# Optimization experiments

Hardware: AMD Instinct MI355X
Metric: run time of the kernel (lower is better)

The kernel has to match this reference:

```python
import jax, jax.numpy as jnp
import numpy as np

N_NODES = 50000
N_EDGES = 800000
IN_DIM = 100
HID = 128
OUT = 128
EPS = 1e-5


def setup_inputs() -> dict:
    key = jax.random.key(0)
    ks = jax.random.split(key, 12)
    x = jax.random.normal(ks[0], (N_NODES, IN_DIM), dtype=jnp.float32)
    edge_index = jax.random.randint(ks[1], (2, N_EDGES), 0, N_NODES, dtype=jnp.int32)
    def lin(k, i, o):
        return jax.random.normal(k, (i, o), dtype=jnp.float32) * (1.0 / np.sqrt(i))
    return {
        "x": x,
        "edge_index": edge_index,
        "W_l0": lin(ks[2], IN_DIM, HID),  # neighbor transform, layer 0
        "b_l0": jnp.zeros((HID,), jnp.float32),
        "W_r0": lin(ks[3], IN_DIM, HID),  # root transform, layer 0
        "gamma0": jnp.ones((HID,), jnp.float32),
        "beta0": jnp.zeros((HID,), jnp.float32),
        "W_l1": lin(ks[4], HID, OUT),
        "b_l1": jnp.zeros((OUT,), jnp.float32),
        "W_r1": lin(ks[5], HID, OUT),
        "gamma1": jnp.ones((OUT,), jnp.float32),
        "beta1": jnp.zeros((OUT,), jnp.float32),
    }


def _sage_conv(x, edge_index, W_l, b_l, W_r):
    # PyG SAGEConv (mean aggr): out = lin_l(mean_{j->i} x_j) + lin_r(x_i)
    src, dst = edge_index[0], edge_index[1]
    n = x.shape[0]
    msg_sum = jax.ops.segment_sum(x[src], dst, num_segments=n)        # [N, d_in]
    cnt = jax.ops.segment_sum(jnp.ones((src.shape[0],), x.dtype), dst, num_segments=n)
    agg = msg_sum / jnp.maximum(cnt, 1.0)[:, None]
    return agg @ W_l + b_l + x @ W_r


def _batch_norm(x, gamma, beta):
    # BatchNorm1d with batch statistics (training-mode math, biased var)
    mean = x.mean(axis=0)
    var = x.var(axis=0)
    return gamma * (x - mean) / jnp.sqrt(var + EPS) + beta


def reference(x, edge_index, W_l0, b_l0, W_r0, gamma0, beta0, W_l1, b_l1, W_r1, gamma1, beta1):
    # Layer 0: SAGEConv -> BN -> ReLU (dropout off for determinism)
    h = _sage_conv(x, edge_index, W_l0, b_l0, W_r0)
    h = jax.nn.relu(_batch_norm(h, gamma0, beta0))
    # Layer 1 (last): SAGEConv -> BN
    h = _sage_conv(h, edge_index, W_l1, b_l1, W_r1)
    return _batch_norm(h, gamma1, beta1)
```

## Files before the change

### kernel.cpp

```cpp
#include <hip/hip_runtime.h>
#include <hip/hip_bf16.h>

#define N_NODES 50000
#define N_EDGES 800000
#define NPAD    50048
#define IN_DIM  100
#define HID     128
#define BN_EPS  1e-5f

#define BSHIFT  6
#define BUCKS   782
#define BSTRIDE 2048
#define BCAP    2048
#define NSLICE  16

typedef unsigned int uint;
typedef unsigned short u16;
typedef __attribute__((ext_vector_type(8))) unsigned short us8;
typedef __attribute__((ext_vector_type(8))) short s8;
typedef __attribute__((ext_vector_type(16))) float f16v;

__device__ __forceinline__ u16 f2bf(float f) {
    uint u = __builtin_bit_cast(uint, f);
    uint r = (u + 0x7FFFu + ((u >> 16) & 1u)) >> 16;
    return (u16)r;
}
__device__ __forceinline__ uint pack2(float a, float b) {
    return (uint)f2bf(a) | ((uint)f2bf(b) << 16);
}
__device__ __forceinline__ float bflo(uint p) { return __builtin_bit_cast(float, p << 16); }
__device__ __forceinline__ float bfhi(uint p) { return __builtin_bit_cast(float, p & 0xFFFF0000u); }

__global__ void init_cursor(int* __restrict__ bcursor) {
    int b = blockIdx.x * 256 + threadIdx.x;
    if (b < BUCKS) bcursor[b] = b * BSTRIDE;
}

__global__ __launch_bounds__(1024) void bucket_scatter_blk(
    const int* __restrict__ src, const int* __restrict__ dst,
    int* __restrict__ bcursor, uint* __restrict__ ebuf) {
    __shared__ int h[BUCKS];
    __shared__ int gb[BUCKS];
    int t = threadIdx.x;
    for (int i = t; i < BUCKS; i += 1024) h[i] = 0;
    __syncthreads();
    int base = blockIdx.x * 8192;
    int myb[8]; uint myv[8];
    #pragma unroll
    for (int r = 0; r < 8; ++r) {
        int e = base + r * 1024 + t;
        int b = -1; uint val = 0;
        if (e < N_EDGES) {
            int d = dst[e];
            b = d >> BSHIFT;
            val = (uint)src[e] | ((uint)(d & 63) << 16);
            atomicAdd(&h[b], 1);
        }
        myb[r] = b; myv[r] = val;
    }
    __syncthreads();
    for (int i = t; i < BUCKS; i += 1024) {
        int c = h[i];
        gb[i] = c ? atomicAdd(&bcursor[i], c) : 0;
        h[i] = 0;
    }
    __syncthreads();
    #pragma unroll
    for (int r = 0; r < 8; ++r) {
        int b = myb[r];
        if (b >= 0) {
            int pos = gb[b] + atomicAdd(&h[b], 1);
            ebuf[pos] = myv[r];
        }
    }
}

__global__ void cast_x_kernel(const float* __restrict__ x, u16* __restrict__ xb) {
    int idx = blockIdx.x * blockDim.x + threadIdx.x;
    if (idx >= NPAD * 128) return;
    int row = idx >> 7, k = idx & 127;
    float v = (row < N_NODES && k < IN_DIM) ? x[row * IN_DIM + k] : 0.f;
    xb[idx] = f2bf(v);
}

__global__ void cast_w_kernel(const float* __restrict__ W_l0, const float* __restrict__ W_r0,
                              const float* __restrict__ W_l1, const float* __restrict__ W_r1,
                              u16* __restrict__ d) {
    int w = blockIdx.y;
    const float* s = (w == 0) ? W_l0 : (w == 1) ? W_r0 : (w == 2) ? W_l1 : W_r1;
    int Ks = (w < 2) ? IN_DIM : HID;
    int idx = blockIdx.x * 256 + threadIdx.x;
    int n = idx >> 7, k = idx & 127;
    float v = (k < Ks) ? s[k * 128 + n] : 0.f;
    d[w * 16384 + idx] = f2bf(v);
}

template <int WRITE_BF16>
__global__ __launch_bounds__(512) void agg_gemm(
    const uint* __restrict__ ebuf, const int* __restrict__ bcursor,
    const u16* __restrict__ X,
    const u16* __restrict__ WtL, const u16* __restrict__ WtR,
    const float* __restrict__ bias,
    float* __restrict__ outf, u16* __restrict__ outb,
    float* __restrict__ gstats) {
    __shared__ u16 Aagg[64][136];
    __shared__ uint eL[BCAP];
    __shared__ u16 srcL[BCAP];
    __shared__ int cnt[64], ro[65], cur[64];
    __shared__ float s1L[128], s2L[128];

    int b = blockIdx.x;
    int t = threadIdx.x;
    int row0 = b * 64;
    int wave = t >> 6, lane = t & 63;
    int quad = lane >> 4, sub = lane & 15;

    int n = bcursor[b] - b * BSTRIDE;
    if (n > BCAP) n = BCAP;
    if (t < 64) cnt[t] = 0;
    if (t < 128) { s1L[t] = 0.f; s2L[t] = 0.f; }
    __syncthreads();
    for (int i = t; i < n; i += 512) {
        uint p = ebuf[b * BSTRIDE + i];
        eL[i] = p;
        atomicAdd(&cnt[p >> 16], 1);
    }
    __syncthreads();
    if (t < 64) {
        int v = cnt[t];
        int s = v;
        #pragma unroll
        for (int off = 1; off < 64; off <<= 1) {
            int u = __shfl_up(s, off, 64);
            if (t >= off) s += u;
        }
        ro[t] = s - v;
        cur[t] = s - v;
        if (t == 63) ro[64] = s;
    }
    __syncthreads();
    for (int i = t; i < n; i += 512) {
        uint p = eL[i];
        int pos = atomicAdd(&cur[p >> 16], 1);
        srcL[pos] = (u16)(p & 0xFFFFu);
    }
    __syncthreads();

    #pragma unroll
    for (int ni = 0; ni < 8; ++ni) {
        int nl = wave * 8 + ni;
        int node = row0 + nl;
        if (node >= N_NODES) {
            if (quad == 0) *(uint4*)&Aagg[nl][sub * 8] = make_uint4(0, 0, 0, 0);
            continue;
        }
        int rb = ro[nl], re = ro[nl + 1];
        float a0 = 0.f, a1 = 0.f, a2 = 0.f, a3 = 0.f;
        float a4 = 0.f, a5 = 0.f, a6 = 0.f, a7 = 0.f;
        int e = rb;
        for (; e + 16 <= re; e += 16) {
            int s0 = srcL[e + quad];
            int s1 = srcL[e + 4 + quad];
            int s2 = srcL[e + 8 + quad];
            int s3 = srcL[e + 12 + quad];
            uint4 v0 = ((const uint4*)(X + (size_t)s0 * 128))[sub];
            uint4 v1 = ((const uint4*)(X + (size_t)s1 * 128))[sub];
            uint4 v2 = ((const uint4*)(X + (size_t)s2 * 128))[sub];
            uint4 v3 = ((const uint4*)(X + (size_t)s3 * 128))[sub];
            a0 += (bflo(v0.x) + bflo(v1.x)) + (bflo(v2.x) + bflo(v3.x));
            a1 += (bfhi(v0.x) + bfhi(v1.x)) + (bfhi(v2.x) + bfhi(v3.x));
            a2 += (bflo(v0.y) + bflo(v1.y)) + (bflo(v2.y) + bflo(v3.y));
            a3 += (bfhi(v0.y) + bfhi(v1.y)) + (bfhi(v2.y) + bfhi(v3.y));
            a4 += (bflo(v0.z) + bflo(v1.z)) + (bflo(v2.z) + bflo(v3.z));
            a5 += (bfhi(v0.z) + bfhi(v1.z)) + (bfhi(v2.z) + bfhi(v3.z));
            a6 += (bflo(v0.w) + bflo(v1.w)) + (bflo(v2.w) + bflo(v3.w));
            a7 += (bfhi(v0.w) + bfhi(v1.w)) + (bfhi(v2.w) + bfhi(v3.w));
        }
        for (; e + 8 <= re; e += 8) {
            int s0 = srcL[e + quad];
            int s1 = srcL[e + 4 + quad];
            uint4 v0 = ((const uint4*)(X + (size_t)s0 * 128))[sub];
            uint4 v1 = ((const uint4*)(X + (size_t)s1 * 128))[sub];
            a0 += bflo(v0.x) + bflo(v1.x);
            a1 += bfhi(v0.x) + bfhi(v1.x);
            a2 += bflo(v0.y) + bflo(v1.y);
            a3 += bfhi(v0.y) + bfhi(v1.y);
            a4 += bflo(v0.z) + bflo(v1.z);
            a5 += bfhi(v0.z) + bfhi(v1.z);
            a6 += bflo(v0.w) + bflo(v1.w);
            a7 += bfhi(v0.w) + bfhi(v1.w);
        }
        for (; e < re; e += 4) {
            int ee = e + quad;
            if (ee < re) {
                int s0 = srcL[ee];
                uint4 v0 = ((const uint4*)(X + (size_t)s0 * 128))[sub];
                a0 += bflo(v0.x); a1 += bfhi(v0.x);
                a2 += bflo(v0.y); a3 += bfhi(v0.y);
                a4 += bflo(v0.z); a5 += bfhi(v0.z);
                a6 += bflo(v0.w); a7 += bfhi(v0.w);
            }
        }
        #pragma unroll
        for (int m = 16; m <= 32; m <<= 1) {
            a0 += __shfl_xor(a0, m, 64); a1 += __shfl_xor(a1, m, 64);
            a2 += __shfl_xor(a2, m, 64); a3 += __shfl_xor(a3, m, 64);
            a4 += __shfl_xor(a4, m, 64); a5 += __shfl_xor(a5, m, 64);
            a6 += __shfl_xor(a6, m, 64); a7 += __shfl_xor(a7, m, 64);
        }
        if (quad == 0) {
            float inv = 1.0f / fmaxf((float)(re - rb), 1.0f);
            uint4 o;
            o.x = pack2(a0 * inv, a1 * inv);
            o.y = pack2(a2 * inv, a3 * inv);
            o.z = pack2(a4 * inv, a5 * inv);
            o.w = pack2(a6 * inv, a7 * inv);
            *(uint4*)&Aagg[nl][sub * 8] = o;
        }
    }
    __syncthreads();

    int m31 = lane & 31;
    int kh  = lane >> 5;
    int rm = (wave & 1) * 32;
    int cn = (wave >> 1) * 32;
    f16v acc = (f16v)0.f;

    {
        s8 a_nxt = *(const s8*)&Aagg[rm + m31][kh * 8];
        s8 b_nxt = *(const s8*)(WtL + (cn + m31) * 128 + kh * 8);
        #pragma unroll
        for (int ks = 0; ks < 8; ++ks) {
            s8 a_cur = a_nxt, b_cur = b_nxt;
            if (ks < 7) {
                a_nxt = *(const s8*)&Aagg[rm + m31][(ks + 1) * 16 + kh * 8];
                b_nxt = *(const s8*)(WtL + (cn + m31) * 128 + (ks + 1) * 16 + kh * 8);
            }
            acc = __builtin_amdgcn_mfma_f32_32x32x16_bf16(a_cur, b_cur, acc, 0, 0, 0);
        }
    }
    {
        const u16* xrow = X + (size_t)(row0 + rm + m31) * 128;
        s8 a_nxt = *(const s8*)(xrow + kh * 8);
        s8 b_nxt = *(const s8*)(WtR + (cn + m31) * 128 + kh * 8);
        #pragma unroll
        for (int ks = 0; ks < 8; ++ks) {
            s8 a_cur = a_nxt, b_cur = b_nxt;
            if (ks < 7) {
                a_nxt = *(const s8*)(xrow + (ks + 1) * 16 + kh * 8);
                b_nxt = *(const s8*)(WtR + (cn + m31) * 128 + (ks + 1) * 16 + kh * 8);
            }
            acc = __builtin_amdgcn_mfma_f32_32x32x16_bf16(a_cur, b_cur, acc, 0, 0, 0);
        }
    }

    {
        int col = cn + m31;
        float bv = bias[col];
        float s1 = 0.f, s2 = 0.f;
        #pragma unroll
        for (int reg = 0; reg < 16; ++reg) {
            int rowin = (reg & 3) + 8 * (reg >> 2) + 4 * kh;
            int row = row0 + rm + rowin;
            if (row < N_NODES) {
                float v = acc[reg] + bv;
                if (WRITE_BF16)
                    outb[(size_t)row * 128 + col] = f2bf(v);
                else
                    outf[(size_t)row * 128 + col] = v;
                s1 += v;
                s2 = fmaf(v, v, s2);
            }
        }
        s1 += __shfl_xor(s1, 32, 64);
        s2 += __shfl_xor(s2, 32, 64);
        if (lane < 32) {
            atomicAdd(&s1L[col], s1);
            atomicAdd(&s2L[col], s2);
        }
    }
    __syncthreads();
    int slice = b & (NSLICE - 1);
    if (t < 128) {
        atomicAdd(&gstats[slice * 256 + t], s1L[t]);
        atomicAdd(&gstats[slice * 256 + 128 + t], s2L[t]);
    }
}

__global__ void bn_relu_inplace(u16* __restrict__ hb,
                                const float* __restrict__ gstats,
                                const float* __restrict__ gamma,
                                const float* __restrict__ beta,
                                float inv_n, int totalv) {
    __shared__ float ss[256];
    int t = threadIdx.x;
    if (t < 128) {
        float m = 0.f, q = 0.f;
        #pragma unroll
        for (int s = 0; s < NSLICE; ++s) {
            m += gstats[s * 256 + t];
            q += gstats[s * 256 + 128 + t];
        }
        float mean = m * inv_n;
        float var = q * inv_n - mean * mean;
        float inv = 1.0f / sqrtf(var + BN_EPS);
        float sc = gamma[t] * inv;
        ss[t] = sc;
        ss[128 + t] = beta[t] - mean * sc;
    }
    __syncthreads();
    for (int i = blockIdx.x * 256 + t; i < totalv; i += gridDim.x * 256) {
        int cg = (i & 15) * 8;
        uint4 p = ((const uint4*)hb)[i];
        float4 scA = *(const float4*)&ss[cg];
        float4 scB = *(const float4*)&ss[cg + 4];
        float4 shA = *(const float4*)&ss[128 + cg];
        float4 shB = *(const float4*)&ss[128 + cg + 4];
        float r0 = fmaxf(fmaf(bflo(p.x), scA.x, shA.x), 0.f);
        float r1 = fmaxf(fmaf(bfhi(p.x), scA.y, shA.y), 0.f);
        float r2 = fmaxf(fmaf(bflo(p.y), scA.z, shA.z), 0.f);
        float r3 = fmaxf(fmaf(bfhi(p.y), scA.w, shA.w), 0.f);
        float r4 = fmaxf(fmaf(bflo(p.z), scB.x, shB.x), 0.f);
        float r5 = fmaxf(fmaf(bfhi(p.z), scB.y, shB.y), 0.f);
        float r6 = fmaxf(fmaf(bflo(p.w), scB.z, shB.z), 0.f);
        float r7 = fmaxf(fmaf(bfhi(p.w), scB.w, shB.w), 0.f);
        uint4 o;
        o.x = pack2(r0, r1);
        o.y = pack2(r2, r3);
        o.z = pack2(r4, r5);
        o.w = pack2(r6, r7);
        ((uint4*)hb)[i] = o;
    }
}

__global__ void bn_apply_kernel(float* __restrict__ h,
                                const float* __restrict__ gstats,
                                const float* __restrict__ gamma,
                                const float* __restrict__ beta,
                                float inv_n, int total4) {
    __shared__ float ss[256];
    int t = threadIdx.x;
    if (t < 128) {
        float m = 0.f, q = 0.f;
        #pragma unroll
        for (int s = 0; s < NSLICE; ++s) {
            m += gstats[s * 256 + t];
            q += gstats[s * 256 + 128 + t];
        }
        float mean = m * inv_n;
        float var = q * inv_n - mean * mean;
        float inv = 1.0f / sqrtf(var + BN_EPS);
        float sc = gamma[t] * inv;
        ss[t] = sc;
        ss[128 + t] = beta[t] - mean * sc;
    }
    __syncthreads();
    for (int i = blockIdx.x * 256 + t; i < total4; i += gridDim.x * 256) {
        int cg = i & 31;
        float4 v = ((float4*)h)[i];
        float4 sc = *(const float4*)&ss[cg * 4];
        float4 sh = *(const float4*)&ss[128 + cg * 4];
        v.x = fmaf(v.x, sc.x, sh.x);
        v.y = fmaf(v.y, sc.y, sh.y);
        v.z = fmaf(v.z, sc.z, sh.z);
        v.w = fmaf(v.w, sc.w, sh.w);
        ((float4*)h)[i] = v;
    }
}

extern "C" void kernel_launch(void* const* d_in, const int* in_sizes, int n_in,
                              void* d_out, int out_size, void* d_ws, size_t ws_size,
                              hipStream_t stream) {
    const float* x      = (const float*)d_in[0];
    const int*   ei     = (const int*)d_in[1];
    const float* W_l0   = (const float*)d_in[2];
    const float* b_l0   = (const float*)d_in[3];
    const float* W_r0   = (const float*)d_in[4];
    const float* gamma0 = (const float*)d_in[5];
    const float* beta0  = (const float*)d_in[6];
    const float* W_l1   = (const float*)d_in[7];
    const float* b_l1   = (const float*)d_in[8];
    const float* W_r1   = (const float*)d_in[9];
    const float* gamma1 = (const float*)d_in[10];
    const float* beta1  = (const float*)d_in[11];

    const int* src = ei;
    const int* dst = ei + N_EDGES;

    char* w = (char*)d_ws;
    auto alloc = [&](size_t bytes) {
        void* p = (void*)w;
        w += (bytes + 255) & ~(size_t)255;
        return p;
    };
    char* zbase    = w;
    float* gstats0 = (float*)alloc(sizeof(float) * NSLICE * 256);
    float* gstats1 = (float*)alloc(sizeof(float) * NSLICE * 256);
    size_t zbytes  = (size_t)(w - zbase);

    int* bcursor   = (int*)alloc(sizeof(int) * BUCKS);
    uint* ebuf     = (uint*)alloc(sizeof(uint) * BUCKS * BSTRIDE);
    u16* xb        = (u16*)alloc(sizeof(u16) * (size_t)NPAD * 128);
    u16* hb        = (u16*)alloc(sizeof(u16) * (size_t)NPAD * 128);
    u16* Wt        = (u16*)alloc(sizeof(u16) * 4 * 16384);
    float* outp    = (float*)d_out;

    hipMemsetAsync(zbase, 0, zbytes, stream);

    const float inv_n = 1.0f / (float)N_NODES;
    const int total4 = N_NODES * HID / 4;
    const int totalv = N_NODES * HID / 8;

    init_cursor<<<(BUCKS + 255) / 256, 256, 0, stream>>>(bcursor);
    bucket_scatter_blk<<<(N_EDGES + 8191) / 8192, 1024, 0, stream>>>(src, dst, bcursor, ebuf);
    cast_x_kernel<<<(NPAD * 128 + 255) / 256, 256, 0, stream>>>(x, xb);
    cast_w_kernel<<<dim3(64, 4), 256, 0, stream>>>(W_l0, W_r0, W_l1, W_r1, Wt);

    agg_gemm<1><<<BUCKS, 512, 0, stream>>>(ebuf, bcursor, xb, Wt, Wt + 16384, b_l0,
                                           nullptr, hb, gstats0);
    bn_relu_inplace<<<1024, 256, 0, stream>>>(hb, gstats0, gamma0, beta0, inv_n, totalv);

    agg_gemm<0><<<BUCKS, 512, 0, stream>>>(ebuf, bcursor, hb, Wt + 2 * 16384, Wt + 3 * 16384,
                                           b_l1, outp, nullptr, gstats1);
    bn_apply_kernel<<<2048, 256, 0, stream>>>(outp, gstats1, gamma1, beta1, inv_n, total4);
}
```

Measured before the change: 232.9 us.

## Assign one node per 16-lane group in gather, fuse casts, drop cursor init

```diff
diff --git a/kernel.cpp b/kernel.cpp
--- a/kernel.cpp
+++ b/kernel.cpp
@@ -30,11 +30,6 @@
 }
 __device__ __forceinline__ float bflo(uint p) { return __builtin_bit_cast(float, p << 16); }
 __device__ __forceinline__ float bfhi(uint p) { return __builtin_bit_cast(float, p & 0xFFFF0000u); }
-
-__global__ void init_cursor(int* __restrict__ bcursor) {
-    int b = blockIdx.x * 256 + threadIdx.x;
-    if (b < BUCKS) bcursor[b] = b * BSTRIDE;
-}
 
 __global__ __launch_bounds__(1024) void bucket_scatter_blk(
     const int* __restrict__ src, const int* __restrict__ dst,
@@ -61,7 +56,7 @@
     __syncthreads();
     for (int i = t; i < BUCKS; i += 1024) {
         int c = h[i];
-        gb[i] = c ? atomicAdd(&bcursor[i], c) : 0;
+        gb[i] = c ? (i * BSTRIDE + atomicAdd(&bcursor[i], c)) : 0;
         h[i] = 0;
     }
     __syncthreads();
@@ -75,24 +70,25 @@
     }
 }
 
-__global__ void cast_x_kernel(const float* __restrict__ x, u16* __restrict__ xb) {
-    int idx = blockIdx.x * blockDim.x + threadIdx.x;
-    if (idx >= NPAD * 128) return;
-    int row = idx >> 7, k = idx & 127;
-    float v = (row < N_NODES && k < IN_DIM) ? x[row * IN_DIM + k] : 0.f;
-    xb[idx] = f2bf(v);
-}
-
-__global__ void cast_w_kernel(const float* __restrict__ W_l0, const float* __restrict__ W_r0,
-                              const float* __restrict__ W_l1, const float* __restrict__ W_r1,
-                              u16* __restrict__ d) {
-    int w = blockIdx.y;
+__global__ void cast_all(const float* __restrict__ x,
+                         const float* __restrict__ W_l0, const float* __restrict__ W_r0,
+                         const float* __restrict__ W_l1, const float* __restrict__ W_r1,
+                         u16* __restrict__ xb, u16* __restrict__ Wt) {
+    int idx = blockIdx.x * 256 + threadIdx.x;
+    if (idx < NPAD * 128) {
+        int row = idx >> 7, k = idx & 127;
+        float v = (row < N_NODES && k < IN_DIM) ? x[row * IN_DIM + k] : 0.f;
+        xb[idx] = f2bf(v);
+        return;
+    }
+    int i2 = idx - NPAD * 128;
+    if (i2 >= 4 * 16384) return;
+    int w = i2 >> 14, i3 = i2 & 16383;
     const float* s = (w == 0) ? W_l0 : (w == 1) ? W_r0 : (w == 2) ? W_l1 : W_r1;
     int Ks = (w < 2) ? IN_DIM : HID;
-    int idx = blockIdx.x * 256 + threadIdx.x;
-    int n = idx >> 7, k = idx & 127;
+    int n = i3 >> 7, k = i3 & 127;
     float v = (k < Ks) ? s[k * 128 + n] : 0.f;
-    d[w * 16384 + idx] = f2bf(v);
+    Wt[i2] = f2bf(v);
 }
 
 template <int WRITE_BF16>
@@ -115,7 +111,7 @@
     int wave = t >> 6, lane = t & 63;
     int quad = lane >> 4, sub = lane & 15;
 
-    int n = bcursor[b] - b * BSTRIDE;
+    int n = bcursor[b];
     if (n > BCAP) n = BCAP;
     if (t < 64) cnt[t] = 0;
     if (t < 128) { s1L[t] = 0.f; s2L[t] = 0.f; }
@@ -146,23 +142,16 @@
     }
     __syncthreads();
 
+    int nl0 = (wave * 4 + quad) * 2;
     #pragma unroll
-    for (int ni = 0; ni < 8; ++ni) {
-        int nl = wave * 8 + ni;
-        int node = row0 + nl;
-        if (node >= N_NODES) {
-            if (quad == 0) *(uint4*)&Aagg[nl][sub * 8] = make_uint4(0, 0, 0, 0);
-            continue;
-        }
+    for (int g = 0; g < 2; ++g) {
+        int nl = nl0 + g;
         int rb = ro[nl], re = ro[nl + 1];
         float a0 = 0.f, a1 = 0.f, a2 = 0.f, a3 = 0.f;
         float a4 = 0.f, a5 = 0.f, a6 = 0.f, a7 = 0.f;
         int e = rb;
-        for (; e + 16 <= re; e += 16) {
-            int s0 = srcL[e + quad];
-            int s1 = srcL[e + 4 + quad];
-            int s2 = srcL[e + 8 + quad];
-            int s3 = srcL[e + 12 + quad];
+        for (; e + 4 <= re; e += 4) {
+            int s0 = srcL[e], s1 = srcL[e + 1], s2 = srcL[e + 2], s3 = srcL[e + 3];
             uint4 v0 = ((const uint4*)(X + (size_t)s0 * 128))[sub];
             uint4 v1 = ((const uint4*)(X + (size_t)s1 * 128))[sub];
             uint4 v2 = ((const uint4*)(X + (size_t)s2 * 128))[sub];
@@ -176,47 +165,20 @@
             a6 += (bflo(v0.w) + bflo(v1.w)) + (bflo(v2.w) + bflo(v3.w));
             a7 += (bfhi(v0.w) + bfhi(v1.w)) + (bfhi(v2.w) + bfhi(v3.w));
         }
-        for (; e + 8 <= re; e += 8) {
-            int s0 = srcL[e + quad];
-            int s1 = srcL[e + 4 + quad];
-            uint4 v0 = ((const uint4*)(X + (size_t)s0 * 128))[sub];
-            uint4 v1 = ((const uint4*)(X + (size_t)s1 * 128))[sub];
-            a0 += bflo(v0.x) + bflo(v1.x);
-            a1 += bfhi(v0.x) + bfhi(v1.x);
-            a2 += bflo(v0.y) + bflo(v1.y);
-            a3 += bfhi(v0.y) + bfhi(v1.y);
-            a4 += bflo(v0.z) + bflo(v1.z);
-            a5 += bfhi(v0.z) + bfhi(v1.z);
-            a6 += bflo(v0.w) + bflo(v1.w);
-            a7 += bfhi(v0.w) + bfhi(v1.w);
-        }
-        for (; e < re; e += 4) {
-            int ee = e + quad;
-            if (ee < re) {
-                int s0 = srcL[ee];
-                uint4 v0 = ((const uint4*)(X + (size_t)s0 * 128))[sub];
-                a0 += bflo(v0.x); a1 += bfhi(v0.x);
-                a2 += bflo(v0.y); a3 += bfhi(v0.y);
-                a4 += bflo(v0.z); a5 += bfhi(v0.z);
-                a6 += bflo(v0.w); a7 += bfhi(v0.w);
-            }
-        }
-        #pragma unroll
-        for (int m = 16; m <= 32; m <<= 1) {
-            a0 += __shfl_xor(a0, m, 64); a1 += __shfl_xor(a1, m, 64);
-            a2 += __shfl_xor(a2, m, 64); a3 += __shfl_xor(a3, m, 64);
-            a4 += __shfl_xor(a4, m, 64); a5 += __shfl_xor(a5, m, 64);
-            a6 += __shfl_xor(a6, m, 64); a7 += __shfl_xor(a7, m, 64);
-        }
-        if (quad == 0) {
-            float inv = 1.0f / fmaxf((float)(re - rb), 1.0f);
-            uint4 o;
-            o.x = pack2(a0 * inv, a1 * inv);
-            o.y = pack2(a2 * inv, a3 * inv);
-            o.z = pack2(a4 * inv, a5 * inv);
-            o.w = pack2(a6 * inv, a7 * inv);
-            *(uint4*)&Aagg[nl][sub * 8] = o;
-        }
+        for (; e < re; ++e) {
+            uint4 v0 = ((const uint4*)(X + (size_t)srcL[e] * 128))[sub];
+            a0 += bflo(v0.x); a1 += bfhi(v0.x);
+            a2 += bflo(v0.y); a3 += bfhi(v0.y);
+            a4 += bflo(v0.z); a5 += bfhi(v0.z);
+            a6 += bflo(v0.w); a7 += bfhi(v0.w);
+        }
+        float inv = 1.0f / fmaxf((float)(re - rb), 1.0f);
+        uint4 o;
+        o.x = pack2(a0 * inv, a1 * inv);
+        o.y = pack2(a2 * inv, a3 * inv);
+        o.z = pack2(a4 * inv, a5 * inv);
+        o.w = pack2(a6 * inv, a7 * inv);
+        *(uint4*)&Aagg[nl][sub * 8] = o;
     }
     __syncthreads();
 
@@ -396,9 +358,9 @@
     char* zbase    = w;
     float* gstats0 = (float*)alloc(sizeof(float) * NSLICE * 256);
     float* gstats1 = (float*)alloc(sizeof(float) * NSLICE * 256);
+    int* bcursor   = (int*)alloc(sizeof(int) * BUCKS);
     size_t zbytes  = (size_t)(w - zbase);
 
-    int* bcursor   = (int*)alloc(sizeof(int) * BUCKS);
     uint* ebuf     = (uint*)alloc(sizeof(uint) * BUCKS * BSTRIDE);
     u16* xb        = (u16*)alloc(sizeof(u16) * (size_t)NPAD * 128);
     u16* hb        = (u16*)alloc(sizeof(u16) * (size_t)NPAD * 128);
@@ -410,11 +372,10 @@
     const float inv_n = 1.0f / (float)N_NODES;
     const int total4 = N_NODES * HID / 4;
     const int totalv = N_NODES * HID / 8;
-
-    init_cursor<<<(BUCKS + 255) / 256, 256, 0, stream>>>(bcursor);
+    const int castN = NPAD * 128 + 4 * 16384;
+
     bucket_scatter_blk<<<(N_EDGES + 8191) / 8192, 1024, 0, stream>>>(src, dst, bcursor, ebuf);
-    cast_x_kernel<<<(NPAD * 128 + 255) / 256, 256, 0, stream>>>(x, xb);
-    cast_w_kernel<<<dim3(64, 4), 256, 0, stream>>>(W_l0, W_r0, W_l1, W_r1, Wt);
+    cast_all<<<(castN + 255) / 256, 256, 0, stream>>>(x, W_l0, W_r0, W_l1, W_r1, xb, Wt);
 
     agg_gemm<1><<<BUCKS, 512, 0, stream>>>(ebuf, bcursor, xb, Wt, Wt + 16384, b_l0,
                                            nullptr, hb, gstats0);
```

Measured after the change: 230.3 us. Within noise of the previous version (-1.1%).
